# Performance work log

Measured on AMD Instinct MI355X. Metric: run time of the kernel, lower is better.

Reference implementation:

```python
import jax, jax.numpy as jnp
import numpy as np

N = 100000   # nodes
E = 800000   # edges
G = 64       # graphs in batch
DIMS = [1, 128, 256, 512]


def _graph_conv(x, src, dst, W_rel, b_rel, W_root):
    # PyG GraphConv: out = lin_rel(sum_{j in N(i)} x_j) + lin_root(x_i)
    agg = jax.ops.segment_sum(x[src], dst, num_segments=x.shape[0])  # [N, d_in]
    return agg @ W_rel + b_rel + x @ W_root  # [N, d_out]


def setup_inputs() -> dict:
    key = jax.random.key(0)
    ks = jax.random.split(key, 16)
    x = jax.random.normal(ks[0], (N, DIMS[0]), dtype=jnp.float32)
    src = jax.random.randint(ks[1], (E,), 0, N, dtype=jnp.int32)
    dst = jax.random.randint(ks[2], (E,), 0, N, dtype=jnp.int32)
    edge_index = jnp.stack([src, dst])  # [2, E]
    batch = jnp.sort(jax.random.randint(ks[3], (N,), 0, G, dtype=jnp.int32))
    params = {}
    for i in range(3):
        d_in, d_out = DIMS[i], DIMS[i + 1]
        s = 1.0 / np.sqrt(d_in)
        params[f"W_rel{i+1}"] = jax.random.uniform(ks[4 + 3 * i], (d_in, d_out), minval=-s, maxval=s, dtype=jnp.float32)
        params[f"b_rel{i+1}"] = jax.random.uniform(ks[5 + 3 * i], (d_out,), minval=-s, maxval=s, dtype=jnp.float32)
        params[f"W_root{i+1}"] = jax.random.uniform(ks[6 + 3 * i], (d_in, d_out), minval=-s, maxval=s, dtype=jnp.float32)
    return {"x": x, "edge_index": edge_index, "batch": batch, **params}


def reference(x, edge_index, batch,
              W_rel1, b_rel1, W_root1,
              W_rel2, b_rel2, W_root2,
              W_rel3, b_rel3, W_root3):
    src, dst = edge_index[0], edge_index[1]
    h = jax.nn.relu(_graph_conv(x, src, dst, W_rel1, b_rel1, W_root1))
    h = jax.nn.relu(_graph_conv(h, src, dst, W_rel2, b_rel2, W_root2))
    h = _graph_conv(h, src, dst, W_rel3, b_rel3, W_root3)  # [N, 512]
    # global mean pool over graphs
    counts = jax.ops.segment_sum(jnp.ones((N,), dtype=h.dtype), batch, num_segments=G)
    pooled = jax.ops.segment_sum(h, batch, num_segments=G) / jnp.maximum(counts, 1.0)[:, None]  # [G, 512]
    # F.normalize: L2-normalize along dim=1 with eps=1e-12
    norm = jnp.linalg.norm(pooled, axis=1, keepdims=True)
    return pooled / jnp.maximum(norm, 1e-12)
```

## Files before the change

### kernel.cpp

```cpp
#include <hip/hip_runtime.h>

#define N_NODES 100000
#define N_EDGES 800000
#define NG      64
#define NPAD    100096

constexpr size_t OFF_AGG1P = 0;
constexpr size_t OFF_ROW  = OFF_AGG1P + 800256;
constexpr size_t OFF_CUR  = OFF_ROW  + 400128;
constexpr size_t OFF_PART = OFF_CUR  + 400128;
constexpr size_t OFF_CSR  = OFF_PART + 512;
constexpr size_t OFF_XCAT = OFF_CSR  + 3200000;
constexpr size_t OFF_MT   = OFF_XCAT;
constexpr size_t OFF_MTB  = OFF_XCAT + 25624576;
constexpr size_t OFF_H2T  = OFF_XCAT + (size_t)NPAD*256*2;
constexpr size_t OFF_WT   = OFF_H2T  + (size_t)NPAD*256*2;
constexpr size_t OFF_PCAT = OFF_WT   + 256*256*2;
constexpr size_t OFF_CNT  = OFF_PCAT + 128*256*4;

typedef __attribute__((ext_vector_type(8))) short bf16x8;
typedef __attribute__((ext_vector_type(8))) unsigned short u16x8;
typedef __attribute__((ext_vector_type(4))) unsigned short u16x4;
typedef __attribute__((ext_vector_type(4))) float f32x4;

__device__ __forceinline__ float bfu2f(unsigned short u) {
    return __uint_as_float(((unsigned)u) << 16);
}
__device__ __forceinline__ unsigned short f2bfu(float f) {
    unsigned u = __float_as_uint(f);
    unsigned r = (u + 0x7FFFu + ((u >> 16) & 1u)) >> 16;
    return (unsigned short)r;
}

__device__ __forceinline__ void load_lds16(const void* g, void* l) {
    __builtin_amdgcn_global_load_lds(
        (const __attribute__((address_space(1))) unsigned int*)g,
        (__attribute__((address_space(3))) unsigned int*)l, 16, 0, 0);
}

#define PK_MASK ((1LL << 44) - 1)
__device__ __forceinline__ float pk_agg(long long v) {
    long long dg = v >> 44;
    return (float)((v & PK_MASK) - (dg << 24)) * (1.f / 1048576.f);
}
__device__ __forceinline__ int pk_deg(long long v) { return (int)(v >> 44); }

__global__ void k_edge1(const float* __restrict__ x, const int* __restrict__ src,
                        const int* __restrict__ dst, unsigned long long* __restrict__ agg1p,
                        int* __restrict__ rank) {
    int e = blockIdx.x * 256 + threadIdx.x;
    if (e >= N_EDGES) return;
    int s = src[e], d = dst[e];
    long long fixed = (long long)lrintf(x[s] * 1048576.f);
    unsigned long long add = (1ULL << 44) + (unsigned long long)(fixed + (1LL << 24));
    unsigned long long old = atomicAdd(&agg1p[d], add);
    rank[e] = (int)(old >> 44);
}

__global__ void k_h1(const long long* __restrict__ agg1p, const float* __restrict__ x,
                     const float* __restrict__ Wr1, const float* __restrict__ Wo1,
                     const float* __restrict__ br1, unsigned short* __restrict__ xcat) {
    int gid = blockIdx.x * 256 + threadIdx.x;
    if (gid >= NPAD * 128) return;
    int i = gid >> 7, d = gid & 127;
    float v = 0.f;
    if (i < N_NODES) {
        float a = pk_agg(agg1p[i]);
        v = fmaxf(fmaf(a, Wr1[d], fmaf(x[i], Wo1[d], br1[d])), 0.f);
    }
    xcat[(size_t)i * 256 + 128 + d] = f2bfu(v);
}

__global__ __launch_bounds__(1024) void k_scanA(const long long* __restrict__ agg1p, int* rowst, int* part) {
    __shared__ int sm[1024];
    int t = threadIdx.x, i = blockIdx.x * 1024 + t;
    int v = (i < N_NODES) ? pk_deg(agg1p[i]) : 0;
    sm[t] = v; __syncthreads();
    for (int o = 1; o < 1024; o <<= 1) {
        int y = (t >= o) ? sm[t - o] : 0;
        __syncthreads();
        sm[t] += y;
        __syncthreads();
    }
    if (i < N_NODES) rowst[i] = sm[t] - v;
    if (t == 1023) part[blockIdx.x] = sm[t];
}
__global__ void k_scanB(int* part) {
    __shared__ int sm[128];
    int t = threadIdx.x;
    int v = (t < 98) ? part[t] : 0;
    sm[t] = v; __syncthreads();
    for (int o = 1; o < 128; o <<= 1) {
        int y = (t >= o) ? sm[t - o] : 0;
        __syncthreads();
        sm[t] += y;
        __syncthreads();
    }
    if (t < 98) part[t] = sm[t] - v;
}
__global__ void k_scanC(int* rowst, const int* __restrict__ part) {
    int i = blockIdx.x * 256 + threadIdx.x;
    if (i >= N_NODES) return;
    rowst[i] += part[i >> 10];
}
__global__ void k_scatter(const int* __restrict__ src, const int* __restrict__ dst,
                          const int* __restrict__ rank, const int* __restrict__ rowst,
                          int* __restrict__ csr) {
    int e = blockIdx.x * 256 + threadIdx.x;
    if (e >= N_EDGES) return;
    csr[rowst[dst[e]] + rank[e]] = src[e];
}

__global__ __launch_bounds__(256) void k_agg2(const long long* __restrict__ agg1p, const float* __restrict__ x,
                                              const int* __restrict__ rowst,
                                              const int* __restrict__ csr,
                                              const float* __restrict__ Wr1, const float* __restrict__ Wo1,
                                              const float* __restrict__ br1, unsigned int* __restrict__ xcat_u32) {
    const int wave = threadIdx.x >> 6, lane = threadIdx.x & 63;
    const int d0 = 2 * lane, d1 = 2 * lane + 1;
    const float u0 = Wr1[d0], u1 = Wr1[d1];
    const float v0 = Wo1[d0], v1 = Wo1[d1];
    const float c0 = br1[d0], c1 = br1[d1];
    int wid = blockIdx.x * 4 + wave;
    int nw = gridDim.x * 4;
    for (int i = wid; i < NPAD; i += nw) {
        float a0 = 0.f, a1 = 0.f;
        if (i < N_NODES) {
            long long pv = agg1p[i];
            int dg = pk_deg(pv), st = rowst[i];
            for (int base = 0; base < dg; base += 64) {
                float av = 0.f, xv = 0.f;
                int e = base + lane;
                if (e < dg) { int s = csr[st + e]; av = pk_agg(agg1p[s]); xv = x[s]; }
                int cnt = min(64, dg - base);
                for (int j = 0; j < cnt; ++j) {
                    float aj = __shfl(av, j);
                    float xj = __shfl(xv, j);
                    a0 += fmaxf(fmaf(aj, u0, fmaf(xj, v0, c0)), 0.f);
                    a1 += fmaxf(fmaf(aj, u1, fmaf(xj, v1, c1)), 0.f);
                }
            }
        }
        unsigned int w = (unsigned)f2bfu(a0) | ((unsigned)f2bfu(a1) << 16);
        xcat_u32[(size_t)i * 128 + lane] = w;
    }
}

__global__ void k_wt(const float* __restrict__ Wr2, const float* __restrict__ Wo2,
                     unsigned short* __restrict__ Wt) {
    int gid = blockIdx.x * 256 + threadIdx.x;
    int k = gid & 255, c = gid >> 8;
    float v = (k < 128) ? Wr2[k * 256 + c] : Wo2[(k - 128) * 256 + c];
    Wt[c * 256 + k] = f2bfu(v);
}

__global__ __launch_bounds__(256) void k_gemm(const short* __restrict__ Xcat, const short* __restrict__ Wt,
                                              const float* __restrict__ b2, unsigned short* __restrict__ h2t) {
    __shared__ short Als[2][4096];
    __shared__ short Bls[2][4096];
    const int wave = threadIdx.x >> 6, lane = threadIdx.x & 63;
    const int r0 = blockIdx.x * 128;
    const int c0 = blockIdx.y * 128;
    const int wr = wave >> 1, wc = wave & 1;

    const int g0 = wave * 64 + lane;
    const int g1 = g0 + 256;
    const int ar0 = g0 >> 2, as0 = (g0 & 3) * 16;
    const int ar1 = g1 >> 2, as1 = (g1 & 3) * 16;
    const char* asrc0 = (const char*)Xcat + (size_t)(r0 + ar0) * 512 + (as0 ^ ((ar0 & 3) << 4));
    const char* asrc1 = (const char*)Xcat + (size_t)(r0 + ar1) * 512 + (as1 ^ ((ar1 & 3) << 4));
    const char* bsrc0 = (const char*)Wt   + (size_t)(c0 + ar0) * 512 + (as0 ^ ((ar0 & 3) << 4));
    const char* bsrc1 = (const char*)Wt   + (size_t)(c0 + ar1) * 512 + (as1 ^ ((ar1 & 3) << 4));
    const int ldsOff0 = wave * 512;
    const int ldsOff1 = wave * 512 + 2048;

    const int lr = lane & 15;
    const int lkb = (lane >> 4) << 4;
    const int swz = (lr & 3) << 4;
    const int abase = ((wr * 64 + lr) * 64 + (lkb ^ swz)) >> 1;
    const int bbase = ((wc * 64 + lr) * 64 + (lkb ^ swz)) >> 1;

    f32x4 acc[4][4];
    #pragma unroll
    for (int m = 0; m < 4; ++m)
        #pragma unroll
        for (int t = 0; t < 4; ++t) acc[m][t] = (f32x4){0.f, 0.f, 0.f, 0.f};

    int koff = 0;
    load_lds16(asrc0, &Als[0][ldsOff0]);
    load_lds16(asrc1, &Als[0][ldsOff1]);
    load_lds16(bsrc0, &Bls[0][ldsOff0]);
    load_lds16(bsrc1, &Bls[0][ldsOff1]);
    __syncthreads();

    #pragma unroll
    for (int step = 0; step < 8; ++step) {
        const int cur = step & 1;
        if (step < 7) {
            koff += 64;
            load_lds16(asrc0 + koff, &Als[cur ^ 1][ldsOff0]);
            load_lds16(asrc1 + koff, &Als[cur ^ 1][ldsOff1]);
            load_lds16(bsrc0 + koff, &Bls[cur ^ 1][ldsOff0]);
            load_lds16(bsrc1 + koff, &Bls[cur ^ 1][ldsOff1]);
        }
        bf16x8 a[4], b[4];
        #pragma unroll
        for (int m = 0; m < 4; ++m) a[m] = *(const bf16x8*)&Als[cur][abase + m * 512];
        #pragma unroll
        for (int t = 0; t < 4; ++t) b[t] = *(const bf16x8*)&Bls[cur][bbase + t * 512];
        #pragma unroll
        for (int m = 0; m < 4; ++m)
            #pragma unroll
            for (int t = 0; t < 4; ++t)
                acc[m][t] = __builtin_amdgcn_mfma_f32_16x16x32_bf16(a[m], b[t], acc[m][t], 0, 0, 0);
        __syncthreads();
    }

    const int rb = (lane >> 4) * 4;
    #pragma unroll
    for (int m = 0; m < 4; ++m) {
        int row = r0 + wr * 64 + m * 16 + rb;
        #pragma unroll
        for (int t = 0; t < 4; ++t) {
            int col = c0 + wc * 64 + t * 16 + lr;
            float bias = b2[col];
            u16x4 w;
            #pragma unroll
            for (int j = 0; j < 4; ++j)
                w[j] = f2bfu(fmaxf(acc[m][t][j] + bias, 0.f));
            *(u16x4*)(h2t + (size_t)col * NPAD + row) = w;
        }
    }
}

__global__ void k_mbedges(const int* __restrict__ src, const int* __restrict__ dst,
                          const int* __restrict__ batch, float* __restrict__ mt) {
    int e = blockIdx.x * 256 + threadIdx.x;
    if (e >= N_EDGES) return;
    int g = batch[dst[e]];
    atomicAdd(&mt[(size_t)g * NPAD + src[e]], 1.f);
}

__global__ __launch_bounds__(256) void k_mbnodes(const int* __restrict__ batch,
                                                 unsigned short* __restrict__ mtb, float* cntf) {
    __shared__ float lc[NG];
    int t = threadIdx.x;
    if (t < NG) lc[t] = 0.f;
    __syncthreads();
    int i = blockIdx.x * 256 + t;
    if (i < N_NODES) {
        int g = batch[i];
        mtb[(size_t)(64 + g) * NPAD + i] = 0x3F80;
        atomicAdd(&lc[g], 1.f);
    }
    __syncthreads();
    if (t < NG) atomicAdd(&cntf[t], lc[t]);
}

__global__ void k_mconv(const float* __restrict__ mt, unsigned short* __restrict__ mtb) {
    size_t base = ((size_t)blockIdx.x * 256 + threadIdx.x) * 8;
    f32x4 a = *(const f32x4*)(mt + base);
    f32x4 b = *(const f32x4*)(mt + base + 4);
    u16x8 w;
    #pragma unroll
    for (int j = 0; j < 4; ++j) { w[j] = f2bfu(a[j]); w[4 + j] = f2bfu(b[j]); }
    *(u16x8*)(mtb + base) = w;
}

__global__ __launch_bounds__(256) void k_pool_gemm(const short* __restrict__ mtb,
                                                   const short* __restrict__ h2t,
                                                   float* __restrict__ pcat) {
    const int wave = threadIdx.x >> 6, lane = threadIdx.x & 63;
    const int m0 = (wave >> 1) * 64;
    const int c0 = blockIdx.y * 64 + (wave & 1) * 32;
    const int lr = lane & 15;
    const int lk = (lane >> 4) << 3;
    const int kbeg = blockIdx.x * 512;
    const int kend = min(kbeg + 512, NPAD);
    f32x4 acc[4][2];
    #pragma unroll
    for (int m = 0; m < 4; ++m)
        #pragma unroll
        for (int t = 0; t < 2; ++t) acc[m][t] = (f32x4){0.f, 0.f, 0.f, 0.f};
    const short* ap = mtb + (size_t)(m0 + lr) * NPAD + lk;
    const short* bp = h2t + (size_t)(c0 + lr) * NPAD + lk;
    for (int k0 = kbeg; k0 < kend; k0 += 32) {
        bf16x8 a[4], b[2];
        #pragma unroll
        for (int m = 0; m < 4; ++m) a[m] = *(const bf16x8*)(ap + (size_t)m * 16 * NPAD + k0);
        #pragma unroll
        for (int t = 0; t < 2; ++t) b[t] = *(const bf16x8*)(bp + (size_t)t * 16 * NPAD + k0);
        #pragma unroll
        for (int m = 0; m < 4; ++m)
            #pragma unroll
            for (int t = 0; t < 2; ++t)
                acc[m][t] = __builtin_amdgcn_mfma_f32_16x16x32_bf16(a[m], b[t], acc[m][t], 0, 0, 0);
    }
    const int rb = (lane >> 4) * 4;
    #pragma unroll
    for (int m = 0; m < 4; ++m) {
        int row = m0 + m * 16 + rb;
        #pragma unroll
        for (int t = 0; t < 2; ++t) {
            int col = c0 + t * 16 + lr;
            #pragma unroll
            for (int j = 0; j < 4; ++j)
                atomicAdd(&pcat[(size_t)(row + j) * 256 + col], acc[m][t][j]);
        }
    }
}

__global__ __launch_bounds__(256) void k_final(const float* __restrict__ Pagg, const float* __restrict__ Ph2,
                                               const float* __restrict__ cntf,
                                               const float* __restrict__ Wr3, const float* __restrict__ br3,
                                               const float* __restrict__ Wo3, float* __restrict__ out) {
    __shared__ float sa[256], sh[256];
    __shared__ float wred[4];
    int g = blockIdx.x, t = threadIdx.x;
    sa[t] = Pagg[g * 256 + t];
    sh[t] = Ph2[g * 256 + t];
    __syncthreads();
    float c0 = 0.f, c1 = 0.f;
    #pragma unroll 4
    for (int k = 0; k < 256; ++k) {
        float a = sa[k], h = sh[k];
        c0 = fmaf(a, Wr3[k * 512 + t], c0);
        c0 = fmaf(h, Wo3[k * 512 + t], c0);
        c1 = fmaf(a, Wr3[k * 512 + t + 256], c1);
        c1 = fmaf(h, Wo3[k * 512 + t + 256], c1);
    }
    float cnt = cntf[g];
    float inv = 1.f / fmaxf(cnt, 1.f);
    float p0 = (c0 + cnt * br3[t]) * inv;
    float p1 = (c1 + cnt * br3[t + 256]) * inv;
    float ss = p0 * p0 + p1 * p1;
    for (int o = 32; o > 0; o >>= 1) ss += __shfl_down(ss, o);
    int lane = t & 63;
    if (lane == 0) wred[t >> 6] = ss;
    __syncthreads();
    float tot = wred[0] + wred[1] + wred[2] + wred[3];
    float inv2 = 1.f / fmaxf(sqrtf(tot), 1e-12f);
    out[g * 512 + t]       = p0 * inv2;
    out[g * 512 + t + 256] = p1 * inv2;
}

extern "C" void kernel_launch(void* const* d_in, const int* in_sizes, int n_in,
                              void* d_out, int out_size, void* d_ws, size_t ws_size,
                              hipStream_t stream) {
    const float* x   = (const float*)d_in[0];
    const int*   ei  = (const int*)d_in[1];
    const int*   bat = (const int*)d_in[2];
    const float* Wr1 = (const float*)d_in[3];
    const float* br1 = (const float*)d_in[4];
    const float* Wo1 = (const float*)d_in[5];
    const float* Wr2 = (const float*)d_in[6];
    const float* br2 = (const float*)d_in[7];
    const float* Wo2 = (const float*)d_in[8];
    const float* Wr3 = (const float*)d_in[9];
    const float* br3 = (const float*)d_in[10];
    const float* Wo3 = (const float*)d_in[11];
    const int* src = ei;
    const int* dst = ei + N_EDGES;

    char* ws = (char*)d_ws;
    unsigned long long* agg1p = (unsigned long long*)(ws + OFF_AGG1P);
    int*            rowst= (int*)(ws + OFF_ROW);
    int*            part = (int*)(ws + OFF_PART);
    int*            csr  = (int*)(ws + OFF_CSR);
    int*            rank = (int*)(ws + OFF_XCAT);
    unsigned short* xcat = (unsigned short*)(ws + OFF_XCAT);
    float*          mt   = (float*)(ws + OFF_MT);
    unsigned short* mtb  = (unsigned short*)(ws + OFF_MTB);
    unsigned short* h2t  = (unsigned short*)(ws + OFF_H2T);
    unsigned short* wt   = (unsigned short*)(ws + OFF_WT);
    float*          pcat = (float*)(ws + OFF_PCAT);
    float*          cntf = (float*)(ws + OFF_CNT);

    hipMemsetAsync(agg1p, 0, (size_t)N_NODES * 8, stream);
    hipMemsetAsync(pcat, 0, 128 * 256 * 4 + 256, stream);

    k_edge1<<<(N_EDGES + 255) / 256, 256, 0, stream>>>(x, src, dst, agg1p, rank);
    k_scanA<<<98, 1024, 0, stream>>>((const long long*)agg1p, rowst, part);
    k_scanB<<<1, 128, 0, stream>>>(part);
    k_scanC<<<(N_NODES + 255) / 256, 256, 0, stream>>>(rowst, part);
    k_scatter<<<(N_EDGES + 255) / 256, 256, 0, stream>>>(src, dst, rank, rowst, csr);
    k_h1<<<(NPAD * 128) / 256, 256, 0, stream>>>((const long long*)agg1p, x, Wr1, Wo1, br1, xcat);
    k_agg2<<<1024, 256, 0, stream>>>((const long long*)agg1p, x, rowst, csr, Wr1, Wo1, br1, (unsigned int*)xcat);
    k_wt<<<256, 256, 0, stream>>>(Wr2, Wo2, wt);
    k_gemm<<<dim3(NPAD / 128, 2), 256, 0, stream>>>((const short*)xcat, (const short*)wt, br2, h2t);

    hipMemsetAsync(ws + OFF_MT, 0, (size_t)64 * NPAD * 4, stream);
    hipMemsetAsync(ws + OFF_MTB + (size_t)64 * NPAD * 2, 0, (size_t)64 * NPAD * 2, stream);
    k_mbedges<<<(N_EDGES + 255) / 256, 256, 0, stream>>>(src, dst, bat, mt);
    k_mbnodes<<<(N_NODES + 255) / 256, 256, 0, stream>>>(bat, mtb, cntf);
    k_mconv<<<(64 * NPAD) / 2048, 256, 0, stream>>>(mt, mtb);
    k_pool_gemm<<<dim3(196, 4), 256, 0, stream>>>((const short*)mtb, (const short*)h2t, pcat);
    k_final<<<NG, 256, 0, stream>>>(pcat, pcat + 64 * 256, cntf, Wr3, br3, Wo3, (float*)d_out);
}
```

Measured before the change: 410.9 us.

## Stage pool GEMM tiles through double-buffered swizzled LDS with full-width blocks

The pooling GEMM used to launch 196x4 blocks that each loaded A and B fragments straight from global memory into registers, so every column block reread the full mtb operand. It now runs 196 blocks of 512 threads, each covering all 256 output columns. A 128x64 A tile and a 256x64 B tile are staged into double-buffered, XOR-swizzled shared memory with async LDS loads, so the next k-slice is prefetched while MFMAs run on the current one. This removes the fourfold reread of mtb and overlaps loads with compute, at the cost of about 96KB of LDS per block, fewer blocks, and more accumulator registers per wave.

```diff
diff --git a/kernel.cpp b/kernel.cpp
--- a/kernel.cpp
+++ b/kernel.cpp
@@ -267,42 +267,86 @@
     *(u16x8*)(mtb + base) = w;
 }
 
-__global__ __launch_bounds__(256) void k_pool_gemm(const short* __restrict__ mtb,
+__global__ __launch_bounds__(512) void k_pool_gemm(const short* __restrict__ mtb,
                                                    const short* __restrict__ h2t,
                                                    float* __restrict__ pcat) {
-    const int wave = threadIdx.x >> 6, lane = threadIdx.x & 63;
-    const int m0 = (wave >> 1) * 64;
-    const int c0 = blockIdx.y * 64 + (wave & 1) * 32;
-    const int lr = lane & 15;
-    const int lk = (lane >> 4) << 3;
+    __shared__ short Als[2][8192];
+    __shared__ short Bls[2][16384];
+    const int tid = threadIdx.x;
+    const int wave = tid >> 6, lane = tid & 63;
+    const int wr = wave >> 2, wc = wave & 3;
     const int kbeg = blockIdx.x * 512;
-    const int kend = min(kbeg + 512, NPAD);
-    f32x4 acc[4][2];
+    const int nsteps = (min(kbeg + 512, NPAD) - kbeg) >> 6;
+
+    const char* asrc[2]; const char* bsrc[4];
+    int aoff[2], boff[4];
+    #pragma unroll
+    for (int c = 0; c < 2; ++c) {
+        int g = c * 512 + tid, r = g >> 3, s = (g & 7) ^ (r & 7);
+        asrc[c] = (const char*)mtb + ((size_t)r * NPAD + kbeg) * 2 + s * 16;
+        aoff[c] = g * 8;
+    }
+    #pragma unroll
+    for (int c = 0; c < 4; ++c) {
+        int g = c * 512 + tid, r = g >> 3, s = (g & 7) ^ (r & 7);
+        bsrc[c] = (const char*)h2t + ((size_t)r * NPAD + kbeg) * 2 + s * 16;
+        boff[c] = g * 8;
+    }
+
+    const int lr = lane & 15, q = lane >> 4;
+    const int sl0 = (q ^ (lr & 7)) * 8;
+    const int sl1 = ((4 + q) ^ (lr & 7)) * 8;
+    int abase[4], bbase[4];
+    #pragma unroll
+    for (int m = 0; m < 4; ++m) abase[m] = (wr * 64 + m * 16 + lr) * 64;
+    #pragma unroll
+    for (int t = 0; t < 4; ++t) bbase[t] = (wc * 64 + t * 16 + lr) * 64;
+
+    f32x4 acc[4][4];
     #pragma unroll
     for (int m = 0; m < 4; ++m)
         #pragma unroll
-        for (int t = 0; t < 2; ++t) acc[m][t] = (f32x4){0.f, 0.f, 0.f, 0.f};
-    const short* ap = mtb + (size_t)(m0 + lr) * NPAD + lk;
-    const short* bp = h2t + (size_t)(c0 + lr) * NPAD + lk;
-    for (int k0 = kbeg; k0 < kend; k0 += 32) {
-        bf16x8 a[4], b[2];
-        #pragma unroll
-        for (int m = 0; m < 4; ++m) a[m] = *(const bf16x8*)(ap + (size_t)m * 16 * NPAD + k0);
-        #pragma unroll
-        for (int t = 0; t < 2; ++t) b[t] = *(const bf16x8*)(bp + (size_t)t * 16 * NPAD + k0);
-        #pragma unroll
-        for (int m = 0; m < 4; ++m)
-            #pragma unroll
-            for (int t = 0; t < 2; ++t)
-                acc[m][t] = __builtin_amdgcn_mfma_f32_16x16x32_bf16(a[m], b[t], acc[m][t], 0, 0, 0);
-    }
-    const int rb = (lane >> 4) * 4;
+        for (int t = 0; t < 4; ++t) acc[m][t] = (f32x4){0.f, 0.f, 0.f, 0.f};
+
+    #pragma unroll
+    for (int c = 0; c < 2; ++c) load_lds16(asrc[c], &Als[0][aoff[c]]);
+    #pragma unroll
+    for (int c = 0; c < 4; ++c) load_lds16(bsrc[c], &Bls[0][boff[c]]);
+    __syncthreads();
+
+    for (int s = 0; s < nsteps; ++s) {
+        const int cur = s & 1;
+        if (s + 1 < nsteps) {
+            int koff = (s + 1) * 128;
+            #pragma unroll
+            for (int c = 0; c < 2; ++c) load_lds16(asrc[c] + koff, &Als[cur ^ 1][aoff[c]]);
+            #pragma unroll
+            for (int c = 0; c < 4; ++c) load_lds16(bsrc[c] + koff, &Bls[cur ^ 1][boff[c]]);
+        }
+        #pragma unroll
+        for (int ksub = 0; ksub < 2; ++ksub) {
+            const int sl = ksub ? sl1 : sl0;
+            bf16x8 a[4], b[4];
+            #pragma unroll
+            for (int m = 0; m < 4; ++m) a[m] = *(const bf16x8*)&Als[cur][abase[m] + sl];
+            #pragma unroll
+            for (int t = 0; t < 4; ++t) b[t] = *(const bf16x8*)&Bls[cur][bbase[t] + sl];
+            #pragma unroll
+            for (int m = 0; m < 4; ++m)
+                #pragma unroll
+                for (int t = 0; t < 4; ++t)
+                    acc[m][t] = __builtin_amdgcn_mfma_f32_16x16x32_bf16(a[m], b[t], acc[m][t], 0, 0, 0);
+        }
+        __syncthreads();
+    }
+
+    const int rb = q * 4;
     #pragma unroll
     for (int m = 0; m < 4; ++m) {
-        int row = m0 + m * 16 + rb;
-        #pragma unroll
-        for (int t = 0; t < 2; ++t) {
-            int col = c0 + t * 16 + lr;
+        int row = wr * 64 + m * 16 + rb;
+        #pragma unroll
+        for (int t = 0; t < 4; ++t) {
+            int col = wc * 64 + t * 16 + lr;
             #pragma unroll
             for (int j = 0; j < 4; ++j)
                 atomicAdd(&pcat[(size_t)(row + j) * 256 + col], acc[m][t][j]);
@@ -394,6 +438,6 @@
     k_mbedges<<<(N_EDGES + 255) / 256, 256, 0, stream>>>(src, dst, bat, mt);
     k_mbnodes<<<(N_NODES + 255) / 256, 256, 0, stream>>>(bat, mtb, cntf);
     k_mconv<<<(64 * NPAD) / 2048, 256, 0, stream>>>(mt, mtb);
-    k_pool_gemm<<<dim3(196, 4), 256, 0, stream>>>((const short*)mtb, (const short*)h2t, pcat);
+    k_pool_gemm<<<196, 512, 0, stream>>>((const short*)mtb, (const short*)h2t, pcat);
     k_final<<<NG, 256, 0, stream>>>(pcat, pcat + 64 * 256, cntf, Wr3, br3, Wo3, (float*)d_out);
 }
```

Measured after the change: 386.5 us. -5.9%, faster.
